# Optimization experiments

Measured on AMD Instinct MI355X. Metric: run time of the kernel, lower is better.

Reference implementation:

```python
import jax, jax.numpy as jnp
import numpy as np

EMBED_DIM = 768
N_HEADS = 12
SEQ_LEN = 577
MAX_REL = 2


def _relative_position_indices(seq_len: int, max_rel: int) -> jnp.ndarray:
    """Static [S, S] int index map into the relative bias table."""
    n_patches = seq_len - 1
    n_per_dim = int(np.sqrt(n_patches))
    n_entries = (2 * max_rel - 1) ** 2
    cls_cls, cls_patch, patch_cls = n_entries, n_entries + 1, n_entries + 2
    idx = np.arange(seq_len)
    qy, qx = (idx - 1) // n_per_dim, (idx - 1) % n_per_dim
    ry = np.clip(qy[:, None] - qy[None, :], -max_rel + 1, max_rel - 1)
    rx = np.clip(qx[:, None] - qx[None, :], -max_rel + 1, max_rel - 1)
    patch_idx = (ry + max_rel - 1) * (2 * max_rel - 1) + (rx + max_rel - 1)
    is_cls = idx == 0
    out = np.where(is_cls[None, :], patch_cls, patch_idx)
    out = np.where(is_cls[:, None], cls_patch, out)
    out = np.where(is_cls[:, None] & is_cls[None, :], cls_cls, out)
    return jnp.asarray(out, dtype=jnp.int32)


def setup_inputs() -> dict:
    key = jax.random.key(0)
    ks = jax.random.split(key, 6)
    e = EMBED_DIM
    scale = 1.0 / np.sqrt(e)
    return {
        "x": jax.random.normal(ks[0], (32, SEQ_LEN, e), dtype=jnp.float32),
        "Wq": jax.random.normal(ks[1], (e, e), dtype=jnp.float32) * scale,
        "Wk": jax.random.normal(ks[2], (e, e), dtype=jnp.float32) * scale,
        "Wv": jax.random.normal(ks[3], (e, e), dtype=jnp.float32) * scale,
        "Wo": jax.random.normal(ks[4], (e, e), dtype=jnp.float32) * scale,
        "bo": jnp.zeros((e,), dtype=jnp.float32),
        "bias_table": jax.random.normal(ks[5], (12,), dtype=jnp.float32) * 0.02,
    }


def reference(x, Wq, Wk, Wv, Wo, bo, bias_table):
    b, s, e = x.shape
    h, d = N_HEADS, e // N_HEADS
    rel_idx = _relative_position_indices(s, MAX_REL)  # [S, S] int32 (static)

    q = (x @ Wq).reshape(b, s, h, d).transpose(0, 2, 1, 3)  # [b,h,s,d]
    k = (x @ Wk).reshape(b, s, h, d).transpose(0, 2, 1, 3)
    v = (x @ Wv).reshape(b, s, h, d).transpose(0, 2, 1, 3)

    scores = jnp.einsum('bhqd,bhkd->bhqk', q, k) / jnp.sqrt(jnp.float32(d))
    bias = jnp.take(bias_table, rel_idx, axis=0)  # [S, S]
    attn = jax.nn.softmax(scores + bias[None, None, :, :], axis=-1)

    out = jnp.einsum('bhqk,bhkd->bhqd', attn, v)
    out = out.transpose(0, 2, 1, 3).reshape(b, s, e)
    return out @ Wo + bo
```

## Files before the change

kernel.cpp:

```cpp
#include <hip/hip_runtime.h>

typedef unsigned short u16;
typedef short short8 __attribute__((ext_vector_type(8)));
typedef float floatx4 __attribute__((ext_vector_type(4)));

#define MFMA16(a, b, c) __builtin_amdgcn_mfma_f32_16x16x32_bf16((a), (b), (c), 0, 0, 0)

__device__ __forceinline__ u16 f2bf(float f) {
  unsigned u = __builtin_bit_cast(unsigned, f);
  u = (u + 0x7fffu + ((u >> 16) & 1u)) >> 16;
  return (u16)u;
}

__device__ __forceinline__ float bf2f(u16 u) {
  return __builtin_bit_cast(float, ((unsigned)u) << 16);
}

__device__ __forceinline__ float exp2hw(float x) {
  float r; asm("v_exp_f32 %0, %1" : "=v"(r) : "v"(x)); return r;
}

__device__ __forceinline__ unsigned cvtpk_bf16(float lo, float hi) {
  unsigned r;
  asm("v_cvt_pk_bf16_f32 %0, %1, %2" : "=v"(r) : "v"(lo), "v"(hi));
  return r;
}

__device__ __forceinline__ float bflo(unsigned u) {
  return __builtin_bit_cast(float, u << 16);
}
__device__ __forceinline__ float bfhi(unsigned u) {
  return __builtin_bit_cast(float, u & 0xffff0000u);
}

__device__ __forceinline__ void gload16(const void* g, void* l) {
  typedef __attribute__((address_space(1))) const void GV;
  typedef __attribute__((address_space(3))) void LV;
  __builtin_amdgcn_global_load_lds((GV*)g, (LV*)l, 16, 0, 0);
}


__global__ void cvt_x_kernel(const float* __restrict__ x, u16* __restrict__ xb, int n4) {
  int i = blockIdx.x * 256 + threadIdx.x;
  if (i >= n4) return;
  float4 v = ((const float4*)x)[i];
  ushort4 r; r.x = f2bf(v.x); r.y = f2bf(v.y); r.z = f2bf(v.z); r.w = f2bf(v.w);
  ((ushort4*)xb)[i] = r;
}

__global__ void cvt_wT_kernel(const float* __restrict__ in, u16* __restrict__ out) {
  __shared__ float tile[64][65];
  const int k0 = blockIdx.x * 64, n0 = blockIdx.y * 64;
  const int t = threadIdx.x;
  const int tr = t >> 6, tc = t & 63;
#pragma unroll
  for (int i = 0; i < 16; ++i) {
    int row = i * 4 + tr;
    tile[row][tc] = in[(size_t)(k0 + row) * 768 + n0 + tc];
  }
  __syncthreads();
#pragma unroll
  for (int i = 0; i < 16; ++i) {
    int row = i * 4 + tr;
    out[(size_t)(n0 + row) * 768 + k0 + tc] = f2bf(tile[tc][row]);
  }
}

__global__ void bias_kernel(const float* __restrict__ table, u16* __restrict__ bp) {
  int idx = blockIdx.x * 256 + threadIdx.x;
  if (idx >= 577 * 76) return;
  int q = idx / 76, kb = idx - q * 76;
  u16 o8[8];
#pragma unroll
  for (int j = 0; j < 8; ++j) {
    int k = kb * 8 + j;
    float v = 0.f;
    if (k <= 576) {
      int id;
      if (q == 0 && k == 0) id = 9;
      else if (q == 0) id = 10;
      else if (k == 0) id = 11;
      else {
        int qy = (q - 1) / 24, qx = (q - 1) % 24;
        int ky = (k - 1) / 24, kx = (k - 1) % 24;
        int ry = qy - ky; ry = ry < -1 ? -1 : (ry > 1 ? 1 : ry);
        int rx = qx - kx; rx = rx < -1 ? -1 : (rx > 1 ? 1 : rx);
        id = (ry + 1) * 3 + (rx + 1);
      }
      v = table[id] * 1.4426950408889634f;
    }
    o8[j] = f2bf(v);
  }
  *(uint4*)(bp + ((size_t)kb * 577 + q) * 8) = *(const uint4*)o8;
}

__global__ void bias576_kernel(const float* __restrict__ table, float* __restrict__ b576) {
  int q = blockIdx.x * 256 + threadIdx.x;
  if (q >= 577) return;
  int id;
  if (q == 0) id = 10;
  else {
    int qy = (q - 1) / 24, qx = (q - 1) % 24;
    int ry = qy - 23; ry = ry < -1 ? -1 : (ry > 1 ? 1 : ry);
    int rx = qx - 23; rx = rx < -1 ? -1 : (rx > 1 ? 1 : rx);
    id = (ry + 1) * 3 + (rx + 1);
  }
  b576[q] = table[id] * 1.4426950408889634f;
}


template <int MODE>
__global__ __launch_bounds__(256) void gemm_kernel(
    const u16* __restrict__ A, const u16* __restrict__ BT,
    const int M, const int NBN,
    float* __restrict__ outF, const float* __restrict__ bvec,
    u16* __restrict__ qarr, u16* __restrict__ karr, u16* __restrict__ vTa) {
  constexpr int K = 768;
  __shared__ __align__(16) u16 smem[17408];
  u16* As = smem;
  u16* Bs = smem + 8192;
  u16* Cs = smem;

  const int nwg = gridDim.x;
  const int q8 = nwg >> 3, r8 = nwg & 7;
  const int xcd = blockIdx.x & 7, jj = blockIdx.x >> 3;
  const int bid = ((xcd < r8) ? xcd * (q8 + 1) : r8 * (q8 + 1) + (xcd - r8) * q8) + jj;

  const int nb = bid % NBN, mb = bid / NBN;
  const int tid = threadIdx.x;
  const int w = tid >> 6, l = tid & 63;
  const int wr = w >> 1, wc = w & 1;
  const int l15 = l & 15, l4 = l >> 4;
  const int m0 = mb * 128, n0 = nb * 128;

  floatx4 acc[4][4];
#pragma unroll
  for (int i = 0; i < 4; ++i)
#pragma unroll
    for (int j = 0; j < 4; ++j) acc[i][j] = 0.f;

  const int trow = tid >> 2;
  const int tk = (tid & 3) * 8;

  auto stage = [&](int buf, int kt) {
    const int k0 = kt * 32;
#pragma unroll
    for (int i = 0; i < 2; ++i) {
      int row = i * 64 + trow;
      int ar = m0 + row; if (ar >= M) ar = M - 1;
      gload16(A + (size_t)ar * K + k0 + tk, &As[buf * 4096 + row * 32 + tk]);
      int br = n0 + row;
      gload16(BT + (size_t)br * K + k0 + tk, &Bs[buf * 4096 + row * 32 + tk]);
    }
  };

  stage(0, 0);
  __syncthreads();
  int cur = 0;
  for (int kt = 0; kt < 24; ++kt) {
    if (kt + 1 < 24) stage(cur ^ 1, kt + 1);
    short8 af[4], bf[4];
#pragma unroll
    for (int mi = 0; mi < 4; ++mi)
      af[mi] = *(const short8*)&As[cur * 4096 + (wr * 64 + mi * 16 + l15) * 32 + l4 * 8];
#pragma unroll
    for (int ni = 0; ni < 4; ++ni)
      bf[ni] = *(const short8*)&Bs[cur * 4096 + (wc * 64 + ni * 16 + l15) * 32 + l4 * 8];
#pragma unroll
    for (int mi = 0; mi < 4; ++mi)
#pragma unroll
      for (int ni = 0; ni < 4; ++ni)
        acc[mi][ni] = MFMA16(af[mi], bf[ni], acc[mi][ni]);
    __syncthreads();
    cur ^= 1;
  }

  if constexpr (MODE == 0) {
    const int proj = nb / 6;
    const int h0 = (nb - proj * 6) * 2;
    const float qs = (proj == 0) ? 0.18033688011112042f : 1.0f;
#pragma unroll
    for (int mi = 0; mi < 4; ++mi)
#pragma unroll
      for (int i = 0; i < 4; ++i) {
        const int rloc = wr * 64 + mi * 16 + l4 * 4 + i;
#pragma unroll
        for (int ni = 0; ni < 4; ++ni) {
          const int cloc = wc * 64 + ni * 16 + l15;
          Cs[rloc * 136 + cloc] = f2bf(acc[mi][ni][i] * qs);
        }
      }
    __syncthreads();

    if (proj < 2) {
      u16* dst = (proj == 0) ? qarr : karr;
      const int r = tid >> 1, half = tid & 1;
      const int mrow = m0 + r;
      if (mrow < M) {
        const int bq = mrow / 577, sq = mrow - bq * 577;
        u16* base = dst + ((size_t)(bq * 12 + h0 + half) * 577 + sq) * 64;
        const u16* src = Cs + r * 136 + half * 64;
#pragma unroll
        for (int j = 0; j < 8; ++j)
          *(uint4*)(base + j * 8) = *(const uint4*)(src + j * 8);
      }
    } else {
      const int rr = tid & 127, chalf = tid >> 7;
      const int mrow = m0 + rr;
      if (mrow < M) {
        const int bq = mrow / 577, sq = mrow - bq * 577;
        u16* vbase = vTa + ((size_t)(bq * 12 + h0 + chalf) * 64) * 608 + sq;
        const u16* src = Cs + rr * 136 + chalf * 64;
#pragma unroll
        for (int dc = 0; dc < 8; ++dc) {
          const short8 vv = *(const short8*)(src + dc * 8);
#pragma unroll
          for (int jjx = 0; jjx < 8; ++jjx)
            vbase[(size_t)(dc * 8 + jjx) * 608] = (u16)vv[jjx];
        }
      }
    }
  } else {
#pragma unroll
    for (int mi = 0; mi < 4; ++mi) {
#pragma unroll
      for (int i = 0; i < 4; ++i) {
        const int mrow = m0 + wr * 64 + mi * 16 + l4 * 4 + i;
        if (mrow >= M) continue;
#pragma unroll
        for (int ni = 0; ni < 4; ++ni) {
          const int ncol = n0 + wc * 64 + ni * 16 + l15;
          outF[(size_t)mrow * 768 + ncol] = acc[mi][ni][i] + bvec[ncol];
        }
      }
    }
  }
}


__global__ __launch_bounds__(256, 2) void attn_kernel(
    const u16* __restrict__ qg, const u16* __restrict__ kg,
    const u16* __restrict__ vT, const u16* __restrict__ bp,
    const float* __restrict__ b576, u16* __restrict__ xa) {
  const int bid = (blockIdx.x & 7) * 240 + (blockIdx.x >> 3);
  const int bh = bid / 5, qblk = bid - bh * 5;
  const int tid = threadIdx.x;
  const int w = tid >> 6, l = tid & 63;
  const int l15 = l & 15, l4 = l >> 4;
  const int qbase = qblk * 128 + w * 32;

  const u16* qh = qg + (size_t)bh * 577 * 64;
  const u16* kh = kg + (size_t)bh * 577 * 64;
  const u16* vh = vT + (size_t)bh * 64 * 608;

  __shared__ u16 Ks[2][64 * 64];
  __shared__ u16 Vs[2][64 * 64];

  const int sr = tid >> 3;
  const int sb = tid & 7;
  const int ss = ((sr & 7) ^ ((2 * (sr >> 3)) & 7)) & 7;
  const int scol = (sb ^ ss) * 8;

  const int sig = ((l15 >> 2) << 3) + (l15 & 3);
  const int s0_ = ((l15 & 3) ^ ((2 * (l15 >> 2)) & 7)) & 7;
  const int s4_ = s0_ ^ 4;
  const int oK00 = sig * 64 + ((l4 ^ s0_) << 3);
  const int oK01 = sig * 64 + (((l4 + 4) ^ s0_) << 3);
  const int oK10 = (sig + 4) * 64 + ((l4 ^ s4_) << 3);
  const int oK11 = (sig + 4) * 64 + (((l4 + 4) ^ s4_) << 3);
  const int oK20 = oK00 + 32 * 64;
  const int oK21 = oK01 + 32 * 64;
  const int oK30 = oK10 + 32 * 64;
  const int oK31 = oK11 + 32 * 64;
  int oV[4][2];
#pragma unroll
  for (int df = 0; df < 4; ++df) {
    const int r = df * 16 + l15;
    const int sv = ((r & 7) ^ ((2 * (r >> 3)) & 7)) & 7;
    oV[df][0] = r * 64 + ((l4 ^ sv) << 3);
    oV[df][1] = r * 64 + (((l4 + 4) ^ sv) << 3);
  }

  short8 qf[2][2];
  int bq[2];
#pragma unroll
  for (int g = 0; g < 2; ++g) {
    int qr = qbase + g * 16 + l15; if (qr > 576) qr = 576;
    bq[g] = qr;
    qf[g][0] = *(const short8*)(qh + qr * 64 + l4 * 8);
    qf[g][1] = *(const short8*)(qh + qr * 64 + 32 + l4 * 8);
  }

  float m[2], lsum[2] = {1.f, 1.f};
  {
    const u16* kp = kh + 576 * 64 + l4 * 8;
    const short8 kA = *(const short8*)(kp);
    const short8 kB = *(const short8*)(kp + 32);
#pragma unroll
    for (int g = 0; g < 2; ++g) {
      float acc = 0.f;
#pragma unroll
      for (int j = 0; j < 8; ++j)
        acc += bf2f((u16)qf[g][0][j]) * bf2f((u16)kA[j]) +
               bf2f((u16)qf[g][1][j]) * bf2f((u16)kB[j]);
      acc += __shfl_xor(acc, 16);
      acc += __shfl_xor(acc, 32);
      m[g] = acc + b576[bq[g]];
    }
  }
  floatx4 o[2][4];
#pragma unroll
  for (int df = 0; df < 4; ++df)
#pragma unroll
    for (int i = 0; i < 4; ++i) {
      const float v5 = bf2f(vh[(size_t)(df * 16 + l4 * 4 + i) * 608 + 576]);
      o[0][df][i] = v5; o[1][df][i] = v5;
    }

  gload16(kh + (size_t)sr * 64 + scol, &Ks[0][sr * 64 + sb * 8]);
  gload16(kh + (size_t)(sr + 32) * 64 + scol, &Ks[0][(sr + 32) * 64 + sb * 8]);
  gload16(vh + (size_t)sr * 608 + scol, &Vs[0][sr * 64 + sb * 8]);
  gload16(vh + (size_t)(sr + 32) * 608 + scol, &Vs[0][(sr + 32) * 64 + sb * 8]);
  __syncthreads();

  for (int t = 0; t < 9; ++t) {
    const int cur = t & 1;
    if (t < 8) {
      const int nk = (t + 1) * 64;
      gload16(kh + (size_t)(nk + sr) * 64 + scol, &Ks[cur ^ 1][sr * 64 + sb * 8]);
      gload16(kh + (size_t)(nk + sr + 32) * 64 + scol, &Ks[cur ^ 1][(sr + 32) * 64 + sb * 8]);
      gload16(vh + (size_t)sr * 608 + nk + scol, &Vs[cur ^ 1][sr * 64 + sb * 8]);
      gload16(vh + (size_t)(sr + 32) * 608 + nk + scol, &Vs[cur ^ 1][(sr + 32) * 64 + sb * 8]);
    }

    const int kba = t * 8 + l4;
    const uint4 ba0 = *(const uint4*)(bp + ((size_t)kba * 577 + bq[0]) * 8);
    const uint4 bb0 = *(const uint4*)(bp + ((size_t)(kba + 4) * 577 + bq[0]) * 8);
    const uint4 ba1 = *(const uint4*)(bp + ((size_t)kba * 577 + bq[1]) * 8);
    const uint4 bb1 = *(const uint4*)(bp + ((size_t)(kba + 4) * 577 + bq[1]) * 8);

    const u16* kb_ = &Ks[cur][0];
    const short8 K00 = *(const short8*)(kb_ + oK00);
    const short8 K01 = *(const short8*)(kb_ + oK01);
    const short8 K10 = *(const short8*)(kb_ + oK10);
    const short8 K11 = *(const short8*)(kb_ + oK11);
    const short8 K20 = *(const short8*)(kb_ + oK20);
    const short8 K21 = *(const short8*)(kb_ + oK21);
    const short8 K30 = *(const short8*)(kb_ + oK30);
    const short8 K31 = *(const short8*)(kb_ + oK31);

    floatx4 sA0[2], sA1[2], sB0[2], sB1[2];
    __builtin_amdgcn_s_setprio(1);
#pragma unroll
    for (int g = 0; g < 2; ++g) {
      floatx4 a0 = 0.f, a1 = 0.f, b0 = 0.f, b1 = 0.f;
      a0 = MFMA16(K00, qf[g][0], a0); a0 = MFMA16(K01, qf[g][1], a0);
      a1 = MFMA16(K10, qf[g][0], a1); a1 = MFMA16(K11, qf[g][1], a1);
      b0 = MFMA16(K20, qf[g][0], b0); b0 = MFMA16(K21, qf[g][1], b0);
      b1 = MFMA16(K30, qf[g][0], b1); b1 = MFMA16(K31, qf[g][1], b1);
      sA0[g] = a0; sA1[g] = a1; sB0[g] = b0; sB1[g] = b1;
    }
    __builtin_amdgcn_s_setprio(0);

    float v_[2][16];
#pragma unroll
    for (int g = 0; g < 2; ++g) {
      const uint4 ba = (g == 0) ? ba0 : ba1;
      const uint4 bb = (g == 0) ? bb0 : bb1;
      v_[g][0] = sA0[g][0] + bflo(ba.x);  v_[g][1] = sA0[g][1] + bfhi(ba.x);
      v_[g][2] = sA0[g][2] + bflo(ba.y);  v_[g][3] = sA0[g][3] + bfhi(ba.y);
      v_[g][4] = sA1[g][0] + bflo(ba.z);  v_[g][5] = sA1[g][1] + bfhi(ba.z);
      v_[g][6] = sA1[g][2] + bflo(ba.w);  v_[g][7] = sA1[g][3] + bfhi(ba.w);
      v_[g][8]  = sB0[g][0] + bflo(bb.x); v_[g][9]  = sB0[g][1] + bfhi(bb.x);
      v_[g][10] = sB0[g][2] + bflo(bb.y); v_[g][11] = sB0[g][3] + bfhi(bb.y);
      v_[g][12] = sB1[g][0] + bflo(bb.z); v_[g][13] = sB1[g][1] + bfhi(bb.z);
      v_[g][14] = sB1[g][2] + bflo(bb.w); v_[g][15] = sB1[g][3] + bfhi(bb.w);
    }

    float vm[2];
#pragma unroll
    for (int g = 0; g < 2; ++g) {
      float a = v_[g][0];
#pragma unroll
      for (int j = 1; j < 16; ++j) a = fmaxf(a, v_[g][j]);
      a = fmaxf(a, __shfl_xor(a, 16));
      a = fmaxf(a, __shfl_xor(a, 32));
      vm[g] = a;
    }

    if (__any((vm[0] > m[0] + 8.f) || (vm[1] > m[1] + 8.f))) {
      const float mn0 = fmaxf(m[0], vm[0]), mn1 = fmaxf(m[1], vm[1]);
      const float sc0 = exp2hw(m[0] - mn0), sc1 = exp2hw(m[1] - mn1);
      lsum[0] *= sc0; lsum[1] *= sc1;
#pragma unroll
      for (int df = 0; df < 4; ++df) { o[0][df] *= sc0; o[1][df] *= sc1; }
      m[0] = mn0; m[1] = mn1;
    }

    union PU { unsigned u[4]; short8 s; };
    PU pA[2], pB[2];
#pragma unroll
    for (int g = 0; g < 2; ++g) {
      float rs = 0.f;
#pragma unroll
      for (int j = 0; j < 16; ++j) { v_[g][j] = exp2hw(v_[g][j] - m[g]); rs += v_[g][j]; }
      rs += __shfl_xor(rs, 16);
      rs += __shfl_xor(rs, 32);
      lsum[g] += rs;
#pragma unroll
      for (int j = 0; j < 4; ++j) {
        pA[g].u[j] = cvtpk_bf16(v_[g][2 * j], v_[g][2 * j + 1]);
        pB[g].u[j] = cvtpk_bf16(v_[g][8 + 2 * j], v_[g][8 + 2 * j + 1]);
      }
    }

    const u16* vb_ = &Vs[cur][0];
    const short8 vA0 = *(const short8*)(vb_ + oV[0][0]);
    const short8 vB0 = *(const short8*)(vb_ + oV[0][1]);
    const short8 vA1 = *(const short8*)(vb_ + oV[1][0]);
    const short8 vB1 = *(const short8*)(vb_ + oV[1][1]);
    const short8 vA2 = *(const short8*)(vb_ + oV[2][0]);
    const short8 vB2 = *(const short8*)(vb_ + oV[2][1]);
    const short8 vA3 = *(const short8*)(vb_ + oV[3][0]);
    const short8 vB3 = *(const short8*)(vb_ + oV[3][1]);

    __builtin_amdgcn_s_setprio(1);
#pragma unroll
    for (int g = 0; g < 2; ++g) {
      o[g][0] = MFMA16(vA0, pA[g].s, o[g][0]); o[g][0] = MFMA16(vB0, pB[g].s, o[g][0]);
      o[g][1] = MFMA16(vA1, pA[g].s, o[g][1]); o[g][1] = MFMA16(vB1, pB[g].s, o[g][1]);
      o[g][2] = MFMA16(vA2, pA[g].s, o[g][2]); o[g][2] = MFMA16(vB2, pB[g].s, o[g][2]);
      o[g][3] = MFMA16(vA3, pA[g].s, o[g][3]); o[g][3] = MFMA16(vB3, pB[g].s, o[g][3]);
    }
    __builtin_amdgcn_s_setprio(0);

    __syncthreads();
  }

  const int b = bh / 12, h = bh - (bh / 12) * 12;
#pragma unroll
  for (int g = 0; g < 2; ++g) {
    const int gq = qbase + g * 16 + l15;
    if (gq < 577) {
      const float inv = 1.f / lsum[g];
      u16* op = xa + ((size_t)(b * 577 + gq)) * 768 + h * 64 + l4 * 4;
#pragma unroll
      for (int d = 0; d < 4; ++d) {
        unsigned w0 = cvtpk_bf16(o[g][d][0] * inv, o[g][d][1] * inv);
        unsigned w1 = cvtpk_bf16(o[g][d][2] * inv, o[g][d][3] * inv);
        *(unsigned*)(op + d * 16) = w0;
        *(unsigned*)(op + d * 16 + 2) = w1;
      }
    }
  }
}


extern "C" void kernel_launch(void* const* d_in, const int* in_sizes, int n_in,
                              void* d_out, int out_size, void* d_ws, size_t ws_size,
                              hipStream_t stream) {
  const float* x  = (const float*)d_in[0];
  const float* Wq = (const float*)d_in[1];
  const float* Wk = (const float*)d_in[2];
  const float* Wv = (const float*)d_in[3];
  const float* Wo = (const float*)d_in[4];
  const float* bo = (const float*)d_in[5];
  const float* bt = (const float*)d_in[6];
  float* out = (float*)d_out;

  char* ws = (char*)d_ws;
  size_t off = 0;
  auto alloc = [&](size_t bytes) {
    void* p = ws + off;
    off += (bytes + 255) & ~(size_t)255;
    return p;
  };
  u16* xb   = (u16*)alloc((size_t)18464 * 768 * 2);
  u16* WT   = (u16*)alloc((size_t)2304 * 768 * 2);
  u16* WoT  = (u16*)alloc((size_t)768 * 768 * 2);
  u16* qa   = (u16*)alloc((size_t)384 * 577 * 64 * 2);
  u16* ka   = (u16*)alloc((size_t)384 * 577 * 64 * 2);
  u16* vT   = (u16*)alloc((size_t)384 * 64 * 608 * 2);
  u16* biasPk = (u16*)alloc((size_t)76 * 577 * 8 * 2);
  float* b576 = (float*)alloc((size_t)577 * 4);
  (void)ws_size; (void)in_sizes; (void)n_in; (void)out_size;

  cvt_x_kernel<<<(18464 * 768 / 4 + 255) / 256, 256, 0, stream>>>(x, xb, 18464 * 768 / 4);
  dim3 tg(12, 12);
  cvt_wT_kernel<<<tg, 256, 0, stream>>>(Wq, WT);
  cvt_wT_kernel<<<tg, 256, 0, stream>>>(Wk, WT + (size_t)768 * 768);
  cvt_wT_kernel<<<tg, 256, 0, stream>>>(Wv, WT + (size_t)2 * 768 * 768);
  cvt_wT_kernel<<<tg, 256, 0, stream>>>(Wo, WoT);
  bias_kernel<<<(577 * 76 + 255) / 256, 256, 0, stream>>>(bt, biasPk);
  bias576_kernel<<<3, 256, 0, stream>>>(bt, b576);

  gemm_kernel<0><<<145 * 18, 256, 0, stream>>>(xb, WT, 18464, 18,
                                               nullptr, nullptr, qa, ka, vT);
  attn_kernel<<<1920, 256, 0, stream>>>(qa, ka, vT, biasPk, b576, xb);
  gemm_kernel<1><<<145 * 6, 256, 0, stream>>>(xb, WoT, 18464, 6,
                                              out, bo, nullptr, nullptr, nullptr);
}
```

Baseline: 247.6 us.

## Enlarge GEMM tiles to 256x256 with 512 threads and prefetch attention bias

Both GEMM kernels move from 128x128 tiles with 256 threads to 256x256 tiles with 512 threads (8 waves, each holding a 128x64 accumulator). The goal is to raise reuse of each staged A/B tile and cut redundant global loads. The QKV epilogue now writes its shared-memory staging tile in two halves to fit LDS. The attention kernel prefetches the relative-bias vectors one iteration ahead and uses tree reductions for the row max and sum to shorten dependency chains. The bigger GEMM tiles raise register and LDS pressure and give fewer workgroups (657 and 219), which risks lower occupancy and poorer load balance across CUs.

```diff
diff --git a/kernel.cpp b/kernel.cpp
--- a/kernel.cpp
+++ b/kernel.cpp
@@ -110,15 +110,15 @@
 
 
 template <int MODE>
-__global__ __launch_bounds__(256) void gemm_kernel(
+__global__ __launch_bounds__(512, 2) void gemm_kernel(
     const u16* __restrict__ A, const u16* __restrict__ BT,
     const int M, const int NBN,
     float* __restrict__ outF, const float* __restrict__ bvec,
     u16* __restrict__ qarr, u16* __restrict__ karr, u16* __restrict__ vTa) {
   constexpr int K = 768;
-  __shared__ __align__(16) u16 smem[17408];
+  __shared__ __align__(16) u16 smem[33792];
   u16* As = smem;
-  u16* Bs = smem + 8192;
+  u16* Bs = smem + 16384;
   u16* Cs = smem;
 
   const int nwg = gridDim.x;
@@ -128,30 +128,28 @@
 
   const int nb = bid % NBN, mb = bid / NBN;
   const int tid = threadIdx.x;
-  const int w = tid >> 6, l = tid & 63;
-  const int wr = w >> 1, wc = w & 1;
+  const int wid = tid >> 6, l = tid & 63;
+  const int wrm = wid >> 2, wcn = wid & 3;
   const int l15 = l & 15, l4 = l >> 4;
-  const int m0 = mb * 128, n0 = nb * 128;
-
-  floatx4 acc[4][4];
-#pragma unroll
-  for (int i = 0; i < 4; ++i)
+  const int m0 = mb * 256, n0 = nb * 256;
+
+  floatx4 acc[8][4];
+#pragma unroll
+  for (int i = 0; i < 8; ++i)
 #pragma unroll
     for (int j = 0; j < 4; ++j) acc[i][j] = 0.f;
 
-  const int trow = tid >> 2;
-  const int tk = (tid & 3) * 8;
+  const int r1 = tid >> 2;
+  const int g1 = (tid & 3) * 8;
 
   auto stage = [&](int buf, int kt) {
-    const int k0 = kt * 32;
-#pragma unroll
-    for (int i = 0; i < 2; ++i) {
-      int row = i * 64 + trow;
-      int ar = m0 + row; if (ar >= M) ar = M - 1;
-      gload16(A + (size_t)ar * K + k0 + tk, &As[buf * 4096 + row * 32 + tk]);
-      int br = n0 + row;
-      gload16(BT + (size_t)br * K + k0 + tk, &Bs[buf * 4096 + row * 32 + tk]);
-    }
+    const int k0 = kt * 32 + g1;
+    int ar0 = m0 + r1;       if (ar0 >= M) ar0 = M - 1;
+    int ar1 = m0 + r1 + 128; if (ar1 >= M) ar1 = M - 1;
+    gload16(A + (size_t)ar0 * K + k0, &As[buf * 8192 + tid * 8]);
+    gload16(A + (size_t)ar1 * K + k0, &As[buf * 8192 + 4096 + tid * 8]);
+    gload16(BT + (size_t)(n0 + r1) * K + k0, &Bs[buf * 8192 + tid * 8]);
+    gload16(BT + (size_t)(n0 + r1 + 128) * K + k0, &Bs[buf * 8192 + 4096 + tid * 8]);
   };
 
   stage(0, 0);
@@ -159,15 +157,15 @@
   int cur = 0;
   for (int kt = 0; kt < 24; ++kt) {
     if (kt + 1 < 24) stage(cur ^ 1, kt + 1);
-    short8 af[4], bf[4];
-#pragma unroll
-    for (int mi = 0; mi < 4; ++mi)
-      af[mi] = *(const short8*)&As[cur * 4096 + (wr * 64 + mi * 16 + l15) * 32 + l4 * 8];
+    short8 af[8], bf[4];
+#pragma unroll
+    for (int mi = 0; mi < 8; ++mi)
+      af[mi] = *(const short8*)&As[cur * 8192 + (wrm * 128 + mi * 16 + l15) * 32 + l4 * 8];
 #pragma unroll
     for (int ni = 0; ni < 4; ++ni)
-      bf[ni] = *(const short8*)&Bs[cur * 4096 + (wc * 64 + ni * 16 + l15) * 32 + l4 * 8];
-#pragma unroll
-    for (int mi = 0; mi < 4; ++mi)
+      bf[ni] = *(const short8*)&Bs[cur * 8192 + (wcn * 64 + ni * 16 + l15) * 32 + l4 * 8];
+#pragma unroll
+    for (int mi = 0; mi < 8; ++mi)
 #pragma unroll
       for (int ni = 0; ni < 4; ++ni)
         acc[mi][ni] = MFMA16(af[mi], bf[ni], acc[mi][ni]);
@@ -176,60 +174,57 @@
   }
 
   if constexpr (MODE == 0) {
-    const int proj = nb / 6;
-    const int h0 = (nb - proj * 6) * 2;
+    const int proj = nb / 3;
+    const int h0 = (nb - proj * 3) * 4;
     const float qs = (proj == 0) ? 0.18033688011112042f : 1.0f;
 #pragma unroll
-    for (int mi = 0; mi < 4; ++mi)
-#pragma unroll
-      for (int i = 0; i < 4; ++i) {
-        const int rloc = wr * 64 + mi * 16 + l4 * 4 + i;
-#pragma unroll
-        for (int ni = 0; ni < 4; ++ni) {
-          const int cloc = wc * 64 + ni * 16 + l15;
-          Cs[rloc * 136 + cloc] = f2bf(acc[mi][ni][i] * qs);
+    for (int p = 0; p < 2; ++p) {
+      __syncthreads();
+      if (wrm == p) {
+#pragma unroll
+        for (int mi = 0; mi < 8; ++mi)
+#pragma unroll
+          for (int i = 0; i < 4; ++i) {
+            const int rloc = mi * 16 + l4 * 4 + i;
+#pragma unroll
+            for (int ni = 0; ni < 4; ++ni)
+              Cs[rloc * 264 + wcn * 64 + ni * 16 + l15] = f2bf(acc[mi][ni][i] * qs);
+          }
+      }
+      __syncthreads();
+      const int r = tid & 127, ch = tid >> 7;
+      const int mrow = m0 + p * 128 + r;
+      if (mrow < M) {
+        const int bq = mrow / 577, sq = mrow - bq * 577;
+        const u16* src = Cs + r * 264 + ch * 64;
+        if (proj < 2) {
+          u16* dst = (proj == 0) ? qarr : karr;
+          u16* base = dst + ((size_t)(bq * 12 + h0 + ch) * 577 + sq) * 64;
+#pragma unroll
+          for (int j2 = 0; j2 < 8; ++j2)
+            *(uint4*)(base + j2 * 8) = *(const uint4*)(src + j2 * 8);
+        } else {
+          u16* vbase = vTa + ((size_t)(bq * 12 + h0 + ch) * 64) * 608 + sq;
+#pragma unroll
+          for (int dc = 0; dc < 8; ++dc) {
+            const short8 vv = *(const short8*)(src + dc * 8);
+#pragma unroll
+            for (int jx = 0; jx < 8; ++jx)
+              vbase[(size_t)(dc * 8 + jx) * 608] = (u16)vv[jx];
+          }
         }
       }
-    __syncthreads();
-
-    if (proj < 2) {
-      u16* dst = (proj == 0) ? qarr : karr;
-      const int r = tid >> 1, half = tid & 1;
-      const int mrow = m0 + r;
-      if (mrow < M) {
-        const int bq = mrow / 577, sq = mrow - bq * 577;
-        u16* base = dst + ((size_t)(bq * 12 + h0 + half) * 577 + sq) * 64;
-        const u16* src = Cs + r * 136 + half * 64;
-#pragma unroll
-        for (int j = 0; j < 8; ++j)
-          *(uint4*)(base + j * 8) = *(const uint4*)(src + j * 8);
-      }
-    } else {
-      const int rr = tid & 127, chalf = tid >> 7;
-      const int mrow = m0 + rr;
-      if (mrow < M) {
-        const int bq = mrow / 577, sq = mrow - bq * 577;
-        u16* vbase = vTa + ((size_t)(bq * 12 + h0 + chalf) * 64) * 608 + sq;
-        const u16* src = Cs + rr * 136 + chalf * 64;
-#pragma unroll
-        for (int dc = 0; dc < 8; ++dc) {
-          const short8 vv = *(const short8*)(src + dc * 8);
-#pragma unroll
-          for (int jjx = 0; jjx < 8; ++jjx)
-            vbase[(size_t)(dc * 8 + jjx) * 608] = (u16)vv[jjx];
-        }
-      }
     }
   } else {
 #pragma unroll
-    for (int mi = 0; mi < 4; ++mi) {
+    for (int mi = 0; mi < 8; ++mi) {
 #pragma unroll
       for (int i = 0; i < 4; ++i) {
-        const int mrow = m0 + wr * 64 + mi * 16 + l4 * 4 + i;
+        const int mrow = m0 + wrm * 128 + mi * 16 + l4 * 4 + i;
         if (mrow >= M) continue;
 #pragma unroll
         for (int ni = 0; ni < 4; ++ni) {
-          const int ncol = n0 + wc * 64 + ni * 16 + l15;
+          const int ncol = n0 + wcn * 64 + ni * 16 + l15;
           outF[(size_t)mrow * 768 + ncol] = acc[mi][ni][i] + bvec[ncol];
         }
       }
@@ -321,23 +316,27 @@
   gload16(kh + (size_t)(sr + 32) * 64 + scol, &Ks[0][(sr + 32) * 64 + sb * 8]);
   gload16(vh + (size_t)sr * 608 + scol, &Vs[0][sr * 64 + sb * 8]);
   gload16(vh + (size_t)(sr + 32) * 608 + scol, &Vs[0][(sr + 32) * 64 + sb * 8]);
+  uint4 bcA0 = *(const uint4*)(bp + ((size_t)l4 * 577 + bq[0]) * 8);
+  uint4 bcB0 = *(const uint4*)(bp + ((size_t)(l4 + 4) * 577 + bq[0]) * 8);
+  uint4 bcA1 = *(const uint4*)(bp + ((size_t)l4 * 577 + bq[1]) * 8);
+  uint4 bcB1 = *(const uint4*)(bp + ((size_t)(l4 + 4) * 577 + bq[1]) * 8);
   __syncthreads();
 
   for (int t = 0; t < 9; ++t) {
     const int cur = t & 1;
+    uint4 nA0 = bcA0, nB0 = bcB0, nA1 = bcA1, nB1 = bcB1;
     if (t < 8) {
       const int nk = (t + 1) * 64;
       gload16(kh + (size_t)(nk + sr) * 64 + scol, &Ks[cur ^ 1][sr * 64 + sb * 8]);
       gload16(kh + (size_t)(nk + sr + 32) * 64 + scol, &Ks[cur ^ 1][(sr + 32) * 64 + sb * 8]);
       gload16(vh + (size_t)sr * 608 + nk + scol, &Vs[cur ^ 1][sr * 64 + sb * 8]);
       gload16(vh + (size_t)(sr + 32) * 608 + nk + scol, &Vs[cur ^ 1][(sr + 32) * 64 + sb * 8]);
-    }
-
-    const int kba = t * 8 + l4;
-    const uint4 ba0 = *(const uint4*)(bp + ((size_t)kba * 577 + bq[0]) * 8);
-    const uint4 bb0 = *(const uint4*)(bp + ((size_t)(kba + 4) * 577 + bq[0]) * 8);
-    const uint4 ba1 = *(const uint4*)(bp + ((size_t)kba * 577 + bq[1]) * 8);
-    const uint4 bb1 = *(const uint4*)(bp + ((size_t)(kba + 4) * 577 + bq[1]) * 8);
+      const int kba = (t + 1) * 8 + l4;
+      nA0 = *(const uint4*)(bp + ((size_t)kba * 577 + bq[0]) * 8);
+      nB0 = *(const uint4*)(bp + ((size_t)(kba + 4) * 577 + bq[0]) * 8);
+      nA1 = *(const uint4*)(bp + ((size_t)kba * 577 + bq[1]) * 8);
+      nB1 = *(const uint4*)(bp + ((size_t)(kba + 4) * 577 + bq[1]) * 8);
+    }
 
     const u16* kb_ = &Ks[cur][0];
     const short8 K00 = *(const short8*)(kb_ + oK00);
@@ -365,8 +364,8 @@
     float v_[2][16];
 #pragma unroll
     for (int g = 0; g < 2; ++g) {
-      const uint4 ba = (g == 0) ? ba0 : ba1;
-      const uint4 bb = (g == 0) ? bb0 : bb1;
+      const uint4 ba = (g == 0) ? bcA0 : bcA1;
+      const uint4 bb = (g == 0) ? bcB0 : bcB1;
       v_[g][0] = sA0[g][0] + bflo(ba.x);  v_[g][1] = sA0[g][1] + bfhi(ba.x);
       v_[g][2] = sA0[g][2] + bflo(ba.y);  v_[g][3] = sA0[g][3] + bfhi(ba.y);
       v_[g][4] = sA1[g][0] + bflo(ba.z);  v_[g][5] = sA1[g][1] + bfhi(ba.z);
@@ -380,9 +379,13 @@
     float vm[2];
 #pragma unroll
     for (int g = 0; g < 2; ++g) {
-      float a = v_[g][0];
-#pragma unroll
-      for (int j = 1; j < 16; ++j) a = fmaxf(a, v_[g][j]);
+      float m0_ = fmaxf(v_[g][0], v_[g][1]),  m1_ = fmaxf(v_[g][2], v_[g][3]);
+      float m2_ = fmaxf(v_[g][4], v_[g][5]),  m3_ = fmaxf(v_[g][6], v_[g][7]);
+      float m4_ = fmaxf(v_[g][8], v_[g][9]),  m5_ = fmaxf(v_[g][10], v_[g][11]);
+      float m6_ = fmaxf(v_[g][12], v_[g][13]), m7_ = fmaxf(v_[g][14], v_[g][15]);
+      float a = fmaxf(fmaxf(m0_, m1_), fmaxf(m2_, m3_));
+      float b = fmaxf(fmaxf(m4_, m5_), fmaxf(m6_, m7_));
+      a = fmaxf(a, b);
       a = fmaxf(a, __shfl_xor(a, 16));
       a = fmaxf(a, __shfl_xor(a, 32));
       vm[g] = a;
@@ -401,9 +404,13 @@
     PU pA[2], pB[2];
 #pragma unroll
     for (int g = 0; g < 2; ++g) {
-      float rs = 0.f;
-#pragma unroll
-      for (int j = 0; j < 16; ++j) { v_[g][j] = exp2hw(v_[g][j] - m[g]); rs += v_[g][j]; }
+#pragma unroll
+      for (int j = 0; j < 16; ++j) v_[g][j] = exp2hw(v_[g][j] - m[g]);
+      float s0 = (v_[g][0] + v_[g][1]) + (v_[g][2] + v_[g][3]);
+      float s1 = (v_[g][4] + v_[g][5]) + (v_[g][6] + v_[g][7]);
+      float s2 = (v_[g][8] + v_[g][9]) + (v_[g][10] + v_[g][11]);
+      float s3 = (v_[g][12] + v_[g][13]) + (v_[g][14] + v_[g][15]);
+      float rs = (s0 + s1) + (s2 + s3);
       rs += __shfl_xor(rs, 16);
       rs += __shfl_xor(rs, 32);
       lsum[g] += rs;
@@ -434,6 +441,7 @@
     }
     __builtin_amdgcn_s_setprio(0);
 
+    bcA0 = nA0; bcB0 = nB0; bcA1 = nA1; bcB1 = nB1;
     __syncthreads();
   }
 
@@ -494,9 +502,9 @@
   bias_kernel<<<(577 * 76 + 255) / 256, 256, 0, stream>>>(bt, biasPk);
   bias576_kernel<<<3, 256, 0, stream>>>(bt, b576);
 
-  gemm_kernel<0><<<145 * 18, 256, 0, stream>>>(xb, WT, 18464, 18,
-                                               nullptr, nullptr, qa, ka, vT);
+  gemm_kernel<0><<<73 * 9, 512, 0, stream>>>(xb, WT, 18464, 9,
+                                             nullptr, nullptr, qa, ka, vT);
   attn_kernel<<<1920, 256, 0, stream>>>(qa, ka, vT, biasPk, b576, xb);
-  gemm_kernel<1><<<145 * 6, 256, 0, stream>>>(xb, WoT, 18464, 6,
-                                              out, bo, nullptr, nullptr, nullptr);
-}
+  gemm_kernel<1><<<73 * 3, 512, 0, stream>>>(xb, WoT, 18464, 3,
+                                             out, bo, nullptr, nullptr, nullptr);
+}
```

Measured after the change: 233.2 us. -5.8%, faster.
